# Kernel tuning notes

Measured on AMD Instinct MI355X. Metric: run time of the kernel, lower is better.

## Reference

```python
import jax, jax.numpy as jnp
import numpy as np

NEARZERO = 1e-5
NMUL = 16
LENF = 15
PARAM_BOUNDS = [
    ("parBETA", 1.0, 6.0), ("parFC", 50.0, 1000.0), ("parK0", 0.05, 0.9),
    ("parK1", 0.01, 0.5), ("parK2", 0.001, 0.2), ("parLP", 0.2, 1.0),
    ("parPERC", 0.0, 10.0), ("parUZL", 0.0, 100.0), ("parTT", -2.5, 2.5),
    ("parCFMAX", 0.5, 10.0), ("parCFR", 0.0, 0.1), ("parCWH", 0.0, 0.2),
    ("parBETAET", 0.3, 5.0), ("parC", 0.0, 1.0),
]
ROUT_A = (0.0, 2.9)
ROUT_B = (0.0, 6.5)


def setup_inputs() -> dict:
    key = jax.random.key(0)
    k1, k2, k3, k4 = jax.random.split(key, 4)
    Nstep, Ngrid = 365, 2000
    return {
        "x_hydro_model": jax.random.uniform(k1, (Nstep, Ngrid, 3), jnp.float32),
        "c_hydro_model": jax.random.normal(k2, (Ngrid, 1), jnp.float32),
        "params_raw": jax.random.uniform(k3, (Nstep, Ngrid, len(PARAM_BOUNDS), NMUL), jnp.float32),
        "conv_params_hydro": jax.random.uniform(k4, (Ngrid, 2), jnp.float32),
    }


def _uh_gamma(a, b, lenF=LENF):
    # a, b: [Ngrid]; returns normalized gamma unit hydrograph [lenF, Ngrid]
    aa = jax.nn.relu(a)[None, :] + 0.1
    theta = jax.nn.relu(b)[None, :] + 0.5
    t = jnp.arange(0.5, float(lenF), dtype=jnp.float32)[:, None]
    denom = jnp.exp(jax.lax.lgamma(aa)) * theta ** aa
    w = (t ** (aa - 1.0)) * jnp.exp(-t / theta) / denom
    return w / w.sum(0)


def _hbv(x_hydro_model, params_raw, conv_params_hydro):
    Nstep, Ngrid, _ = x_hydro_model.shape
    # static parameters: last timestep, scaled to physical bounds -> [Ngrid, NMUL]
    p = {name: params_raw[-1, :, i, :] * (hi - lo) + lo
         for i, (name, lo, hi) in enumerate(PARAM_BOUNDS)}
    # forcings broadcast over the nmul component axis
    Pm = jnp.broadcast_to(x_hydro_model[:, :, 0:1], (Nstep, Ngrid, NMUL))
    Tm = jnp.broadcast_to(x_hydro_model[:, :, 1:2], (Nstep, Ngrid, NMUL))
    PETm = jnp.broadcast_to(x_hydro_model[:, :, 2:3], (Nstep, Ngrid, NMUL))

    s0 = jnp.full((Ngrid, NMUL), 0.001, jnp.float32)
    init = (s0, s0, s0, s0, s0)  # SNOWPACK, MELTWATER, SM, SUZ, SLZ

    def step(state, inp):
        SNOWPACK, MELTWATER, SM, SUZ, SLZ = state
        P, T, PET = inp
        RAIN = jnp.where(T >= p["parTT"], P, 0.0)
        SNOW = jnp.where(T < p["parTT"], P, 0.0)
        SNOWPACK = SNOWPACK + SNOW
        melt = jnp.clip(p["parCFMAX"] * (T - p["parTT"]), 0.0, None)
        melt = jnp.minimum(melt, SNOWPACK)
        MELTWATER = MELTWATER + melt
        SNOWPACK = jnp.maximum(SNOWPACK - melt, NEARZERO)
        refreezing = jnp.clip(p["parCFR"] * p["parCFMAX"] * (p["parTT"] - T), 0.0, None)
        refreezing = jnp.minimum(refreezing, MELTWATER)
        SNOWPACK = SNOWPACK + refreezing
        MELTWATER = jnp.maximum(MELTWATER - refreezing, NEARZERO)
        tosoil = jnp.clip(MELTWATER - p["parCWH"] * SNOWPACK, 0.0, None)
        MELTWATER = jnp.maximum(MELTWATER - tosoil, NEARZERO)
        soil_wetness = jnp.clip((SM / p["parFC"]) ** p["parBETA"], 0.0, 1.0)
        recharge = (RAIN + tosoil) * soil_wetness
        SM = SM + RAIN + tosoil - recharge
        excess = jnp.clip(SM - p["parFC"], 0.0, None)
        SM = jnp.maximum(SM - excess, NEARZERO)
        evapfactor = jnp.clip((SM / (p["parLP"] * p["parFC"])) ** p["parBETAET"], 0.0, 1.0)
        ETact = jnp.minimum(SM, PET * evapfactor)
        SM = jnp.maximum(SM - ETact, NEARZERO)
        capillary = jnp.minimum(SLZ, p["parC"] * SLZ * (1.0 - jnp.clip(SM / p["parFC"], None, 1.0)))
        SM = jnp.maximum(SM + capillary, NEARZERO)
        SLZ = jnp.maximum(SLZ - capillary, NEARZERO)
        SUZ = SUZ + recharge + excess
        PERC = jnp.minimum(SUZ, p["parPERC"])
        SUZ = SUZ - PERC
        Q0 = p["parK0"] * jnp.clip(SUZ - p["parUZL"], 0.0, None)
        SUZ = SUZ - Q0
        Q1 = p["parK1"] * SUZ
        SUZ = SUZ - Q1
        SLZ = SLZ + PERC
        Q2 = p["parK2"] * SLZ
        SLZ = SLZ - Q2
        return (SNOWPACK, MELTWATER, SM, SUZ, SLZ), Q0 + Q1 + Q2

    _, Qsimmu = jax.lax.scan(step, init, (Pm, Tm, PETm))  # [Nstep, Ngrid, NMUL]
    Qsimavg = Qsimmu.mean(-1)                             # [Nstep, Ngrid] (muwts=None)

    # gamma unit-hydrograph routing = per-basin causal grouped conv1d
    tempa = conv_params_hydro[:, 0] * (ROUT_A[1] - ROUT_A[0]) + ROUT_A[0]
    tempb = conv_params_hydro[:, 1] * (ROUT_B[1] - ROUT_B[0]) + ROUT_B[0]
    UH = _uh_gamma(tempa, tempb, LENF)                    # [LENF, Ngrid]
    conv1 = jax.vmap(lambda xg, wg: jnp.convolve(xg, wg)[:Nstep])
    Qsrout = conv1(Qsimavg.T, UH.T).T                     # [Nstep, Ngrid]
    return Qsrout[:, :, None]                             # flow_sim [Nstep, Ngrid, 1]


def reference(x_hydro_model, c_hydro_model, params_raw, conv_params_hydro):
    return _hbv(x_hydro_model, params_raw, conv_params_hydro)
```

## Files before the change

kernel.cpp:

```cpp
#include <hip/hip_runtime.h>


#define LENF 15

__device__ __forceinline__ float flog2(float x) { return __builtin_amdgcn_logf(x); }
__device__ __forceinline__ float fexp2(float x) { return __builtin_amdgcn_exp2f(x); }
__device__ __forceinline__ float fpow(float x, float y) { return fexp2(y * flog2(x)); }

template <int CTRL>
__device__ __forceinline__ float dpp_add(float x) {
    int p = __builtin_amdgcn_update_dpp(0, __float_as_int(x), CTRL, 0xF, 0xF, true);
    return x + __int_as_float(p);
}

__global__ __launch_bounds__(64, 1) void hbv_kernel(
    const float* __restrict__ x,
    const float* __restrict__ praw,
    const float* __restrict__ convp,
    float* __restrict__ out,
    int Nstep, int Ngrid)
{
    const int tid = threadIdx.x;
    const int gl  = tid >> 4;
    const int m   = tid & 15;
    const int g0  = blockIdx.x * 4;
    const int g   = g0 + gl;

    __shared__ float4 lds4[1104];
    __shared__ float  qbuf[366 * 4];
    float* ldsx = (float*)lds4;

    {
        const float4* src = (const float4*)(x + (size_t)g0 * 3);
        const int row4   = (Ngrid * 3) >> 2;
        const int total4 = Nstep * 3;
        float4 tmp[18];
        #pragma unroll
        for (int k = 0; k < 18; ++k) {
            int j = tid + (k << 6);
            if (j < total4) {
                int t = j / 3, q = j - t * 3;
                tmp[k] = src[(size_t)t * row4 + q];
            }
        }
        #pragma unroll
        for (int k = 0; k < 18; ++k) {
            int j = tid + (k << 6);
            if (j < total4) lds4[j] = tmp[k];
        }
    }
    __syncthreads();

    const float lo[14] = {1.0f, 50.0f, 0.05f, 0.01f, 0.001f, 0.2f, 0.0f, 0.0f,
                          -2.5f, 0.5f, 0.0f, 0.0f, 0.3f, 0.0f};
    const float hi[14] = {6.0f, 1000.0f, 0.9f, 0.5f, 0.2f, 1.0f, 10.0f, 100.0f,
                          2.5f, 10.0f, 0.1f, 0.2f, 5.0f, 1.0f};
    float par[14];
    {
        const float* pr = praw + ((size_t)(Nstep - 1) * Ngrid + g) * 14 * 16 + m;
        #pragma unroll
        for (int i = 0; i < 14; ++i)
            par[i] = fmaf(pr[i * 16], hi[i] - lo[i], lo[i]);
    }
    const float pBETA = par[0], pFC = par[1], pK0 = par[2], pK1 = par[3], pK2 = par[4],
                pLP = par[5], pPERC = par[6], pUZL = par[7], pTT = par[8], pCFMAX = par[9],
                pCFR = par[10], pCWH = par[11], pBETAET = par[12], pC = par[13];
    const float invFC    = 1.0f / pFC;
    const float invLPFC  = 1.0f / (pLP * pFC);
    const float cfrcfmax = pCFR * pCFMAX;

    float uh[LENF];
    {
        float a  = convp[g * 2 + 0] * 2.9f;
        float bb = convp[g * 2 + 1] * 6.5f;
        float aa = fmaxf(a, 0.0f) + 0.1f;
        float th = fmaxf(bb, 0.0f) + 0.5f;
        float am1 = aa - 1.0f;
        float c1  = 1.4426950408889634f / th;
        const float L[LENF] = {
            -1.0f, 0.5849625007f, 1.3219280949f, 1.8073549221f, 2.1699250014f,
            2.4594316186f, 2.7004397181f, 2.9068905956f, 3.0874628413f, 3.2479275134f,
            3.3923174228f, 3.5235619561f, 3.6438561898f, 3.7548875022f, 3.8579809951f};
        float s = 0.0f;
        #pragma unroll
        for (int k = 0; k < LENF; ++k) {
            float t = (float)k + 0.5f;
            float w = fexp2(fmaf(am1, L[k], -t * c1));
            uh[k] = w;
            s += w;
        }
        float is = 1.0f / s;
        #pragma unroll
        for (int k = 0; k < LENF; ++k) uh[k] *= is;
    }

    const float NZ = 1e-5f;
    float SNOWPACK = 1e-3f, MELTWATER = 1e-3f, SM = 1e-3f, SUZ = 1e-3f, SLZ = 1e-3f;

    int b = gl * 3;
    float Pc = ldsx[b], Tc = ldsx[b + 1], Ec = ldsx[b + 2];
    float* qrow = qbuf + gl;

    for (int t = 0; t < Nstep; ++t) {
        b += 12;
        float Pn = ldsx[b], Tn = ldsx[b + 1], En = ldsx[b + 2];

        float P = Pc, T = Tc, PET = Ec;
        bool warm  = (T >= pTT);
        float RAIN = warm ? P : 0.0f;
        float SNOW = warm ? 0.0f : P;
        SNOWPACK += SNOW;
        float melt = fminf(fmaxf(pCFMAX * (T - pTT), 0.0f), SNOWPACK);
        MELTWATER += melt;
        SNOWPACK = fmaxf(SNOWPACK - melt, NZ);
        float refr = fminf(fmaxf(cfrcfmax * (pTT - T), 0.0f), MELTWATER);
        SNOWPACK += refr;
        MELTWATER = fmaxf(MELTWATER - refr, NZ);
        float tosoil = fmaxf(fmaf(-pCWH, SNOWPACK, MELTWATER), 0.0f);
        MELTWATER = fmaxf(MELTWATER - tosoil, NZ);
        float sw = fminf(fpow(SM * invFC, pBETA), 1.0f);
        float rt = RAIN + tosoil;
        float recharge = rt * sw;
        SM = SM + rt - recharge;
        float excess = fmaxf(SM - pFC, 0.0f);
        SM = fmaxf(SM - excess, NZ);
        float ev = fminf(fpow(SM * invLPFC, pBETAET), 1.0f);
        float ETact = fminf(SM, PET * ev);
        SM = fmaxf(SM - ETact, NZ);
        float cap = fminf(SLZ, pC * SLZ * (1.0f - fminf(SM * invFC, 1.0f)));
        SM  = fmaxf(SM + cap, NZ);
        SLZ = fmaxf(SLZ - cap, NZ);
        SUZ = SUZ + recharge + excess;
        float perc = fminf(SUZ, pPERC);
        SUZ -= perc;
        float Q0 = pK0 * fmaxf(SUZ - pUZL, 0.0f);
        SUZ -= Q0;
        float Q1 = pK1 * SUZ;
        SUZ -= Q1;
        SLZ += perc;
        float Q2 = pK2 * SLZ;
        SLZ -= Q2;
        float q = Q0 + Q1 + Q2;

        float qs = q;
        qs = dpp_add<0x121>(qs);
        qs = dpp_add<0x122>(qs);
        qs = dpp_add<0x124>(qs);
        qs = dpp_add<0x128>(qs);
        if (m == 0) qrow[t * 4] = qs * 0.0625f;

        Pc = Pn; Tc = Tn; Ec = En;
    }
    __syncthreads();

    const int chunk = (Nstep + 15) >> 4;
    int t0 = m * chunk;
    int t1 = min(t0 + chunk, Nstep);
    float w[LENF];
    #pragma unroll
    for (int k = 0; k < LENF; ++k) {
        int tt = t0 - k;
        w[k] = (tt >= 0) ? qrow[tt * 4] : 0.0f;
    }
    for (int t = t0; t < t1; ++t) {
        float acc = 0.0f;
        #pragma unroll
        for (int k = 0; k < LENF; ++k) acc = fmaf(uh[k], w[k], acc);
        out[(size_t)t * Ngrid + g] = acc;
        #pragma unroll
        for (int k = LENF - 1; k > 0; --k) w[k] = w[k - 1];
        w[0] = (t + 1 < Nstep) ? qrow[(t + 1) * 4] : 0.0f;
    }
}

extern "C" void kernel_launch(void* const* d_in, const int* in_sizes, int n_in,
                              void* d_out, int out_size, void* d_ws, size_t ws_size,
                              hipStream_t stream) {
    const float* x     = (const float*)d_in[0];
    const float* praw  = (const float*)d_in[2];
    const float* convp = (const float*)d_in[3];
    float* out = (float*)d_out;

    int Ngrid = in_sizes[3] / 2;
    int Nstep = in_sizes[0] / (3 * Ngrid);
    int blocks = Ngrid / 4;

    hbv_kernel<<<blocks, 64, 0, stream>>>(x, praw, convp, out, Nstep, Ngrid);
}
```

Measured before the change: 778.9 us.

## Shorten DPP reduction in scan loop, defer partial sums to convolution phase

The serial time loop now does only two DPP adds per step and stores four partial sums per basin. The last reduction stage and the 1/16 scaling move into the convolution phase, which reads them as float4. Forcings are staged as padded float4 rows, the scan is unrolled by two with prefetch, and the staging barrier now sits after the parameter and unit-hydrograph setup so that work overlaps the load. The aim is a shorter per-step latency chain on the serial critical path. The cost is scalar, less coalesced global loads during staging and more shared memory.

```diff
diff --git a/kernel.cpp b/kernel.cpp
--- a/kernel.cpp
+++ b/kernel.cpp
@@ -26,30 +26,15 @@
     const int g0  = blockIdx.x * 4;
     const int g   = g0 + gl;
 
-    __shared__ float4 lds4[1104];
-    __shared__ float  qbuf[366 * 4];
-    float* ldsx = (float*)lds4;
+    __shared__ float fbuf[368 * 16];
+    __shared__ float qbuf[368 * 16];
 
-    {
-        const float4* src = (const float4*)(x + (size_t)g0 * 3);
-        const int row4   = (Ngrid * 3) >> 2;
-        const int total4 = Nstep * 3;
-        float4 tmp[18];
-        #pragma unroll
-        for (int k = 0; k < 18; ++k) {
-            int j = tid + (k << 6);
-            if (j < total4) {
-                int t = j / 3, q = j - t * 3;
-                tmp[k] = src[(size_t)t * row4 + q];
-            }
-        }
-        #pragma unroll
-        for (int k = 0; k < 18; ++k) {
-            int j = tid + (k << 6);
-            if (j < total4) lds4[j] = tmp[k];
-        }
+    for (int j = tid; j < Nstep * 4; j += 64) {
+        int t = j >> 2, gg = j & 3;
+        const float* s = x + ((size_t)t * Ngrid + (g0 + gg)) * 3;
+        float4 v; v.x = s[0]; v.y = s[1]; v.z = s[2]; v.w = 0.0f;
+        *(float4*)(fbuf + t * 16 + gg * 4) = v;
     }
-    __syncthreads();
 
     const float lo[14] = {1.0f, 50.0f, 0.05f, 0.01f, 0.001f, 0.2f, 0.0f, 0.0f,
                           -2.5f, 0.5f, 0.0f, 0.0f, 0.3f, 0.0f};
@@ -94,18 +79,13 @@
         for (int k = 0; k < LENF; ++k) uh[k] *= is;
     }
 
+    __syncthreads();
+
     const float NZ = 1e-5f;
     float SNOWPACK = 1e-3f, MELTWATER = 1e-3f, SM = 1e-3f, SUZ = 1e-3f, SLZ = 1e-3f;
 
-    int b = gl * 3;
-    float Pc = ldsx[b], Tc = ldsx[b + 1], Ec = ldsx[b + 2];
-    float* qrow = qbuf + gl;
-
-    for (int t = 0; t < Nstep; ++t) {
-        b += 12;
-        float Pn = ldsx[b], Tn = ldsx[b + 1], En = ldsx[b + 2];
-
-        float P = Pc, T = Tc, PET = Ec;
+    auto STEP = [&](float4 f, float* qdst) {
+        float P = f.x, T = f.y, PET = f.z;
         bool warm  = (T >= pTT);
         float RAIN = warm ? P : 0.0f;
         float SNOW = warm ? 0.0f : P;
@@ -142,34 +122,55 @@
         SLZ -= Q2;
         float q = Q0 + Q1 + Q2;
 
-        float qs = q;
-        qs = dpp_add<0x121>(qs);
+        float qs = dpp_add<0x121>(q);
         qs = dpp_add<0x122>(qs);
-        qs = dpp_add<0x124>(qs);
-        qs = dpp_add<0x128>(qs);
-        if (m == 0) qrow[t * 4] = qs * 0.0625f;
+        if ((m & 3) == 0) qdst[m >> 2] = qs;
+    };
 
-        Pc = Pn; Tc = Tn; Ec = En;
+    const float4* fv = (const float4*)fbuf + gl;
+    float* qd = qbuf + gl * 4;
+    float4 fA = fv[0];
+    float4 fB = fv[4];
+    int t = 0;
+    for (; t + 2 < Nstep; t += 2) {
+        STEP(fA, qd);
+        fA = fv[(t + 2) * 4];
+        STEP(fB, qd + 16);
+        fB = fv[(t + 3) * 4];
+        qd += 32;
     }
+    STEP(fA, qd);
+    if (t + 1 < Nstep) STEP(fB, qd + 16);
     __syncthreads();
 
     const int chunk = (Nstep + 15) >> 4;
     int t0 = m * chunk;
     int t1 = min(t0 + chunk, Nstep);
+    const float4* qv = (const float4*)qbuf + gl;
     float w[LENF];
     #pragma unroll
     for (int k = 0; k < LENF; ++k) {
         int tt = t0 - k;
-        w[k] = (tt >= 0) ? qrow[tt * 4] : 0.0f;
+        if (tt >= 0) {
+            float4 r = qv[tt * 4];
+            w[k] = ((r.x + r.y) + (r.z + r.w)) * 0.0625f;
+        } else {
+            w[k] = 0.0f;
+        }
     }
-    for (int t = t0; t < t1; ++t) {
+    for (int tt = t0; tt < t1; ++tt) {
         float acc = 0.0f;
         #pragma unroll
         for (int k = 0; k < LENF; ++k) acc = fmaf(uh[k], w[k], acc);
-        out[(size_t)t * Ngrid + g] = acc;
+        out[(size_t)tt * Ngrid + g] = acc;
         #pragma unroll
         for (int k = LENF - 1; k > 0; --k) w[k] = w[k - 1];
-        w[0] = (t + 1 < Nstep) ? qrow[(t + 1) * 4] : 0.0f;
+        if (tt + 1 < Nstep) {
+            float4 r = qv[(tt + 1) * 4];
+            w[0] = ((r.x + r.y) + (r.z + r.w)) * 0.0625f;
+        } else {
+            w[0] = 0.0f;
+        }
     }
 }
 
```

After: 772.7 us. About the same (-0.8%).
